# Kernel optimization log

Hardware: AMD Instinct MI355X
Metric: run time of the kernel (lower is better)

Reference implementation:

```python
import jax, jax.numpy as jnp
import numpy as np

B, N, CI, CO = 2, 64, 32, 32  # batch, n points, Rs_in channels (j), Rs_out channels (i)


def setup_inputs() -> dict:
    key = jax.random.key(0)
    kf, kg, kw = jax.random.split(key, 3)
    features = jax.random.normal(kf, (B, N, N, CI), dtype=jnp.float32)
    geometry = jax.random.normal(kg, (B, N, 3), dtype=jnp.float32)
    # Continuous kernel parameters: linear map from relative vector (xyz) to 6*CO*CI kernel entries
    W = jax.random.normal(kw, (3, 6 * CO * CI), dtype=jnp.float32) / jnp.sqrt(3.0)
    return {"features": features, "geometry": geometry, "W": W, "n_norm": 1}


def reference(features, geometry, W, n_norm):
    z, n = geometry.shape[:2]
    ci = features.shape[-1]
    co = W.shape[1] // (6 * ci)
    # rel[z, a, b] = r_b - r_a  (rb = unsqueeze(1), ra = unsqueeze(2))
    rel = geometry[:, None, :, :] - geometry[:, :, None, :]  # [z, a, b, 3]
    k = jnp.einsum('zabx,xk->zabk', rel, W).reshape(z, n, n, 6 * co, ci)
    k = k / jnp.sqrt(6.0 * (n_norm ** 2))
    k1, k2, k3, k4, k5, k6 = jnp.split(k, 6, axis=3)  # each [z, a, b, i, j]
    # Precompute shared feature reductions over c and d once (fused HBM savings)
    fs = features.sum(axis=2)   # sum over d -> [z, c, j]
    fd = features.sum(axis=1)   # sum over c -> [z, d, j]
    ft = fs.sum(axis=1)         # sum over c,d -> [z, j]
    out = jnp.einsum('zabij,zj->zabi', k1, ft)
    out = out + jnp.einsum('zacij,zcj->zai', k2, fs)[:, :, None, :]
    out = out + jnp.einsum('zadij,zdj->zai', k3, fd)[:, :, None, :]
    out = out + jnp.einsum('zbcij,zcj->zbi', k4, fs)[:, None, :, :]
    out = out + jnp.einsum('zbdij,zdj->zbi', k5, fd)[:, None, :, :]
    out = out + jnp.einsum('zcdij,zcdj->zi', k6, features)[:, None, None, :]
    return out  # [z, a, b, i]
```

## Files before the change

kernel.cpp:

```cpp
#include <hip/hip_runtime.h>
#include <math.h>

#define NZ 2
#define NN 64
#define NCI 32
#define NCO 32

#define PART_Z_STRIDE (32 * 7 * 32)

__device__ __forceinline__ void ld4(const float* __restrict__ p, float* d) {
    const float4 v = *(const float4*)p;
    d[0] = v.x; d[1] = v.y; d[2] = v.z; d[3] = v.w;
}

__global__ __launch_bounds__(256) void k_reduce(const float* __restrict__ feat,
                                                const float* __restrict__ geom,
                                                float* __restrict__ part) {
    const int bid = blockIdx.x;
    const int z = bid >> 5;
    const int s = bid & 31;
    const int tid = threadIdx.x;
    const int cg = tid & 7;
    const int rg = tid >> 3;

    __shared__ float gsh[NN * 3];
    __shared__ float red[32][7][32];

    if (tid < NN * 3) gsh[tid] = geom[z * NN * 3 + tid];
    __syncthreads();

    float ft[4] = {0.f, 0.f, 0.f, 0.f};
    float As[3][4] = {{0.f}};
    float Ad[3][4] = {{0.f}};

    const float* fz = feat + (size_t)z * NN * NN * NCI;
    const int p0 = s * 128 + rg * 4;
    #pragma unroll
    for (int t = 0; t < 4; ++t) {
        const int p = p0 + t;
        float f[4];
        ld4(fz + (size_t)p * NCI + cg * 4, f);
        const int c = p >> 6;
        const int d = p & 63;
        float gc[3], gd[3];
        #pragma unroll
        for (int x = 0; x < 3; ++x) { gc[x] = gsh[c * 3 + x]; gd[x] = gsh[d * 3 + x]; }
        #pragma unroll
        for (int k = 0; k < 4; ++k) {
            ft[k] += f[k];
            #pragma unroll
            for (int x = 0; x < 3; ++x) {
                As[x][k] = fmaf(gc[x], f[k], As[x][k]);
                Ad[x][k] = fmaf(gd[x], f[k], Ad[x][k]);
            }
        }
    }

    const int j0 = cg * 4;
    #pragma unroll
    for (int k = 0; k < 4; ++k) {
        red[rg][0][j0 + k] = ft[k];
        #pragma unroll
        for (int x = 0; x < 3; ++x) {
            red[rg][1 + x][j0 + k] = As[x][k];
            red[rg][4 + x][j0 + k] = Ad[x][k];
        }
    }
    __syncthreads();

    if (tid < 7 * 32) {
        const int q = tid >> 5, jj = tid & 31;
        float sum = 0.f;
        #pragma unroll
        for (int g = 0; g < 32; ++g) sum += red[g][q][jj];
        part[(size_t)z * PART_Z_STRIDE + (s * 7 + q) * 32 + jj] = sum;
    }
}

__global__ __launch_bounds__(256) void k_out(const float* __restrict__ part,
                                             const float* __restrict__ W,
                                             const float* __restrict__ geom,
                                             const int* __restrict__ nnp,
                                             float* __restrict__ out) {
    const int z = blockIdx.x >> 7;
    const int tid = threadIdx.x;

    __shared__ float gsh[NN * 3];
    __shared__ float acc[7][32];
    __shared__ float sQA[3][32], sQB[3][32], gred[3][32], sgam[32];

    if (tid < NN * 3) gsh[tid] = geom[z * NN * 3 + tid];

    if (tid < 7 * 32) {
        const int q = tid >> 5, j = tid & 31;
        const float* pz = part + (size_t)z * PART_Z_STRIDE;
        float sum = 0.f;
        #pragma unroll 8
        for (int sl = 0; sl < 32; ++sl) sum += pz[(sl * 7 + q) * 32 + j];
        acc[q][j] = sum;
    }
    __syncthreads();

    const int v = *nnp;
    const float nn = (v > 0 && v < (1 << 23)) ? (float)v : __int_as_float(v);
    const float scale = 1.0f / sqrtf(6.0f * nn * nn);

    if (tid < 96) {
        const int x = tid >> 5;
        const int i = tid & 31;
        const float* Wp = W + x * 6 * NCO * NCI + i * NCI;
        float q1 = 0.f, q23 = 0.f, q45 = 0.f, gp = 0.f;
        #pragma unroll 2
        for (int j4 = 0; j4 < 8; ++j4) {
            float w[6][4];
            #pragma unroll
            for (int m = 0; m < 6; ++m) ld4(Wp + m * 1024 + j4 * 4, w[m]);
            #pragma unroll
            for (int k = 0; k < 4; ++k) {
                const int j = j4 * 4 + k;
                const float ftj = acc[0][j];
                const float gsj = acc[1 + x][j];
                const float gdj = acc[4 + x][j];
                q1  = fmaf(w[0][k], ftj, q1);
                q23 = fmaf(w[1][k] + w[2][k], ftj, q23);
                q45 = fmaf(w[3][k] + w[4][k], ftj, q45);
                gp  = fmaf(w[1][k] + w[3][k] - w[5][k], gsj, gp);
                gp  = fmaf(w[2][k] + w[4][k] + w[5][k], gdj, gp);
            }
        }
        sQA[x][i] = scale * (q1 + q23);
        sQB[x][i] = scale * (q1 - q45);
        gred[x][i] = gp;
    }
    __syncthreads();
    if (tid < 32) sgam[tid] = scale * (gred[0][tid] + gred[1][tid] + gred[2][tid]);
    __syncthreads();

    const int i0 = (tid & 7) * 4;
    const int ab = ((blockIdx.x & 127) << 5) + (tid >> 3);
    const int a = ab >> 6, b = ab & 63;

    float r[4];
    #pragma unroll
    for (int k = 0; k < 4; ++k) r[k] = sgam[i0 + k];
    #pragma unroll
    for (int x = 0; x < 3; ++x) {
        const float gb = gsh[b * 3 + x];
        const float ga = gsh[a * 3 + x];
        #pragma unroll
        for (int k = 0; k < 4; ++k) {
            r[k] = fmaf(gb, sQB[x][i0 + k], r[k]);
            r[k] = fmaf(-ga, sQA[x][i0 + k], r[k]);
        }
    }
    float4 o; o.x = r[0]; o.y = r[1]; o.z = r[2]; o.w = r[3];
    *(float4*)(out + ((size_t)(z * 4096 + ab)) * 32 + i0) = o;
}

extern "C" void kernel_launch(void* const* d_in, const int* in_sizes, int n_in,
                              void* d_out, int out_size, void* d_ws, size_t ws_size,
                              hipStream_t stream) {
    const float* feat = (const float*)d_in[0];
    const float* geom = (const float*)d_in[1];
    const float* W    = (const float*)d_in[2];
    const int*   nnp  = (const int*)d_in[3];

    float* part = (float*)d_ws;
    float* out  = (float*)d_out;

    k_reduce<<<NZ * 32, 256, 0, stream>>>(feat, geom, part);
    k_out<<<NZ * 128, 256, 0, stream>>>(part, W, geom, nnp, out);
}
```

Measured before the change: 17.25 us.

## Fuse reduce and output kernels with atomics and a grid-wide barrier

Merges the two kernels into one 256-block kernel. Each block reduces its slice of features with wave shuffles, folds its partial sums through the W projection itself, and atomically adds the small QA/QB/gamma tables into workspace. A spin-wait grid barrier then lets all blocks read the finished tables and write the output. This removes a kernel launch and the partial-sum round trip, but adds a memset launch, atomic contention, and relies on all 256 blocks being co-resident to avoid deadlock.

```diff
diff --git a/kernel.cpp b/kernel.cpp
--- a/kernel.cpp
+++ b/kernel.cpp
@@ -5,109 +5,85 @@
 #define NN 64
 #define NCI 32
 #define NCO 32
+#define NBLOCKS 256
 
-#define PART_Z_STRIDE (32 * 7 * 32)
+#define WS_QA  0
+#define WS_QB  192
+#define WS_GAM 384
+#define WS_CTR 448
 
 __device__ __forceinline__ void ld4(const float* __restrict__ p, float* d) {
     const float4 v = *(const float4*)p;
     d[0] = v.x; d[1] = v.y; d[2] = v.z; d[3] = v.w;
 }
 
-__global__ __launch_bounds__(256) void k_reduce(const float* __restrict__ feat,
-                                                const float* __restrict__ geom,
-                                                float* __restrict__ part) {
-    const int bid = blockIdx.x;
-    const int z = bid >> 5;
-    const int s = bid & 31;
-    const int tid = threadIdx.x;
-    const int cg = tid & 7;
-    const int rg = tid >> 3;
+__global__ __launch_bounds__(256) void k_fused(const float* __restrict__ feat,
+                                               const float* __restrict__ geom,
+                                               const float* __restrict__ W,
+                                               const int* __restrict__ nnp,
+                                               float* __restrict__ ws,
+                                               float* __restrict__ out) {
+    const int bid  = blockIdx.x;
+    const int z    = bid >> 7;
+    const int s    = bid & 127;
+    const int tid  = threadIdx.x;
+    const int lane = tid & 63;
+    const int wv   = tid >> 6;
 
     __shared__ float gsh[NN * 3];
-    __shared__ float red[32][7][32];
+    __shared__ float wred[4][7][32];
+    __shared__ float sacc[7][32];
+    __shared__ float stab[224];
 
     if (tid < NN * 3) gsh[tid] = geom[z * NN * 3 + tid];
     __syncthreads();
 
-    float ft[4] = {0.f, 0.f, 0.f, 0.f};
-    float As[3][4] = {{0.f}};
-    float Ad[3][4] = {{0.f}};
+    const int rg = tid >> 3;
+    const int cg = tid & 7;
+    const int p  = s * 32 + rg;
+    const int c  = p >> 6, d = p & 63;
 
-    const float* fz = feat + (size_t)z * NN * NN * NCI;
-    const int p0 = s * 128 + rg * 4;
+    float f[4];
+    ld4(feat + ((size_t)z * 4096 + p) * NCI + cg * 4, f);
+
+    float v[7][4];
     #pragma unroll
-    for (int t = 0; t < 4; ++t) {
-        const int p = p0 + t;
-        float f[4];
-        ld4(fz + (size_t)p * NCI + cg * 4, f);
-        const int c = p >> 6;
-        const int d = p & 63;
-        float gc[3], gd[3];
+    for (int k = 0; k < 4; ++k) v[0][k] = f[k];
+    #pragma unroll
+    for (int x = 0; x < 3; ++x) {
+        const float gc = gsh[c * 3 + x], gd = gsh[d * 3 + x];
         #pragma unroll
-        for (int x = 0; x < 3; ++x) { gc[x] = gsh[c * 3 + x]; gd[x] = gsh[d * 3 + x]; }
+        for (int k = 0; k < 4; ++k) { v[1 + x][k] = gc * f[k]; v[4 + x][k] = gd * f[k]; }
+    }
+    #pragma unroll
+    for (int q = 0; q < 7; ++q)
         #pragma unroll
         for (int k = 0; k < 4; ++k) {
-            ft[k] += f[k];
+            float t = v[q][k];
+            t += __shfl_xor(t, 8);
+            t += __shfl_xor(t, 16);
+            t += __shfl_xor(t, 32);
+            v[q][k] = t;
+        }
+    if (lane < 8) {
+        #pragma unroll
+        for (int q = 0; q < 7; ++q)
             #pragma unroll
-            for (int x = 0; x < 3; ++x) {
-                As[x][k] = fmaf(gc[x], f[k], As[x][k]);
-                Ad[x][k] = fmaf(gd[x], f[k], Ad[x][k]);
-            }
-        }
+            for (int k = 0; k < 4; ++k) wred[wv][q][lane * 4 + k] = v[q][k];
     }
-
-    const int j0 = cg * 4;
-    #pragma unroll
-    for (int k = 0; k < 4; ++k) {
-        red[rg][0][j0 + k] = ft[k];
-        #pragma unroll
-        for (int x = 0; x < 3; ++x) {
-            red[rg][1 + x][j0 + k] = As[x][k];
-            red[rg][4 + x][j0 + k] = Ad[x][k];
-        }
+    __syncthreads();
+    if (tid < 224) {
+        const int q = tid >> 5, j = tid & 31;
+        sacc[q][j] = wred[0][q][j] + wred[1][q][j] + wred[2][q][j] + wred[3][q][j];
     }
     __syncthreads();
 
-    if (tid < 7 * 32) {
-        const int q = tid >> 5, jj = tid & 31;
-        float sum = 0.f;
-        #pragma unroll
-        for (int g = 0; g < 32; ++g) sum += red[g][q][jj];
-        part[(size_t)z * PART_Z_STRIDE + (s * 7 + q) * 32 + jj] = sum;
-    }
-}
-
-__global__ __launch_bounds__(256) void k_out(const float* __restrict__ part,
-                                             const float* __restrict__ W,
-                                             const float* __restrict__ geom,
-                                             const int* __restrict__ nnp,
-                                             float* __restrict__ out) {
-    const int z = blockIdx.x >> 7;
-    const int tid = threadIdx.x;
-
-    __shared__ float gsh[NN * 3];
-    __shared__ float acc[7][32];
-    __shared__ float sQA[3][32], sQB[3][32], gred[3][32], sgam[32];
-
-    if (tid < NN * 3) gsh[tid] = geom[z * NN * 3 + tid];
-
-    if (tid < 7 * 32) {
-        const int q = tid >> 5, j = tid & 31;
-        const float* pz = part + (size_t)z * PART_Z_STRIDE;
-        float sum = 0.f;
-        #pragma unroll 8
-        for (int sl = 0; sl < 32; ++sl) sum += pz[(sl * 7 + q) * 32 + j];
-        acc[q][j] = sum;
-    }
-    __syncthreads();
-
-    const int v = *nnp;
-    const float nn = (v > 0 && v < (1 << 23)) ? (float)v : __int_as_float(v);
-    const float scale = 1.0f / sqrtf(6.0f * nn * nn);
+    const int vn = *nnp;
+    const float nnv = (vn > 0 && vn < (1 << 23)) ? (float)vn : __int_as_float(vn);
+    const float scale = 1.0f / sqrtf(6.0f * nnv * nnv);
 
     if (tid < 96) {
-        const int x = tid >> 5;
-        const int i = tid & 31;
+        const int x = tid >> 5, i = tid & 31;
         const float* Wp = W + x * 6 * NCO * NCI + i * NCI;
         float q1 = 0.f, q23 = 0.f, q45 = 0.f, gp = 0.f;
         #pragma unroll 2
@@ -118,9 +94,9 @@
             #pragma unroll
             for (int k = 0; k < 4; ++k) {
                 const int j = j4 * 4 + k;
-                const float ftj = acc[0][j];
-                const float gsj = acc[1 + x][j];
-                const float gdj = acc[4 + x][j];
+                const float ftj = sacc[0][j];
+                const float gsj = sacc[1 + x][j];
+                const float gdj = sacc[4 + x][j];
                 q1  = fmaf(w[0][k], ftj, q1);
                 q23 = fmaf(w[1][k] + w[2][k], ftj, q23);
                 q45 = fmaf(w[3][k] + w[4][k], ftj, q45);
@@ -128,30 +104,45 @@
                 gp  = fmaf(w[2][k] + w[4][k] + w[5][k], gdj, gp);
             }
         }
-        sQA[x][i] = scale * (q1 + q23);
-        sQB[x][i] = scale * (q1 - q45);
-        gred[x][i] = gp;
+        unsafeAtomicAdd(ws + WS_QA + z * 96 + tid, scale * (q1 + q23));
+        unsafeAtomicAdd(ws + WS_QB + z * 96 + tid, scale * (q1 - q45));
+        unsafeAtomicAdd(ws + WS_GAM + z * 32 + i, scale * gp);
+    }
+    __threadfence();
+    __syncthreads();
+
+    unsigned* ctr = (unsigned*)(ws + WS_CTR);
+    if (tid == 0) {
+        __hip_atomic_fetch_add(ctr, 1u, __ATOMIC_RELEASE, __HIP_MEMORY_SCOPE_AGENT);
+        while (__hip_atomic_load(ctr, __ATOMIC_RELAXED, __HIP_MEMORY_SCOPE_AGENT) < NBLOCKS)
+            __builtin_amdgcn_s_sleep(2);
+        (void)__hip_atomic_load(ctr, __ATOMIC_ACQUIRE, __HIP_MEMORY_SCOPE_AGENT);
     }
     __syncthreads();
-    if (tid < 32) sgam[tid] = scale * (gred[0][tid] + gred[1][tid] + gred[2][tid]);
+
+    if (tid < 96)
+        stab[tid] = __hip_atomic_load(ws + WS_QA + z * 96 + tid,
+                                      __ATOMIC_RELAXED, __HIP_MEMORY_SCOPE_AGENT);
+    else if (tid < 192)
+        stab[tid] = __hip_atomic_load(ws + WS_QB + z * 96 + (tid - 96),
+                                      __ATOMIC_RELAXED, __HIP_MEMORY_SCOPE_AGENT);
+    else if (tid < 224)
+        stab[tid] = __hip_atomic_load(ws + WS_GAM + z * 32 + (tid - 192),
+                                      __ATOMIC_RELAXED, __HIP_MEMORY_SCOPE_AGENT);
     __syncthreads();
 
-    const int i0 = (tid & 7) * 4;
-    const int ab = ((blockIdx.x & 127) << 5) + (tid >> 3);
-    const int a = ab >> 6, b = ab & 63;
-
+    const int pr = tid >> 3, i0 = (tid & 7) * 4;
+    const int ab = s * 32 + pr, a = ab >> 6, b = ab & 63;
     float r[4];
     #pragma unroll
-    for (int k = 0; k < 4; ++k) r[k] = sgam[i0 + k];
+    for (int k = 0; k < 4; ++k) r[k] = stab[192 + i0 + k];
     #pragma unroll
     for (int x = 0; x < 3; ++x) {
-        const float gb = gsh[b * 3 + x];
-        const float ga = gsh[a * 3 + x];
+        const float gb = gsh[b * 3 + x], ga = gsh[a * 3 + x];
         #pragma unroll
-        for (int k = 0; k < 4; ++k) {
-            r[k] = fmaf(gb, sQB[x][i0 + k], r[k]);
-            r[k] = fmaf(-ga, sQA[x][i0 + k], r[k]);
-        }
+        for (int k = 0; k < 4; ++k)
+            r[k] = fmaf(gb, stab[96 + x * 32 + i0 + k],
+                        fmaf(-ga, stab[x * 32 + i0 + k], r[k]));
     }
     float4 o; o.x = r[0]; o.y = r[1]; o.z = r[2]; o.w = r[3];
     *(float4*)(out + ((size_t)(z * 4096 + ab)) * 32 + i0) = o;
@@ -165,9 +156,8 @@
     const float* W    = (const float*)d_in[2];
     const int*   nnp  = (const int*)d_in[3];
 
-    float* part = (float*)d_ws;
-    float* out  = (float*)d_out;
+    hipMemsetAsync(d_ws, 0, 2048, stream);
 
-    k_reduce<<<NZ * 32, 256, 0, stream>>>(feat, geom, part);
-    k_out<<<NZ * 128, 256, 0, stream>>>(part, W, geom, nnp, out);
+    k_fused<<<NBLOCKS, 256, 0, stream>>>(feat, geom, W, nnp,
+                                         (float*)d_ws, (float*)d_out);
 }
```

New measurement: 56.34 us. 3.27x slower.
